# Optimization experiments

Measured on AMD Instinct MI355X. Metric: run time of the kernel, lower is better.

The kernel has to match this reference:

```python
import jax, jax.numpy as jnp
import numpy as np

DIM = 768
HEADS = 12
ROWS = COLS = 24          # 384 // 16
NP = ROWS * COLS          # 576 patches
N = NP + 1                # +1 cls token
NREL = (2 * ROWS - 1) * (2 * COLS - 1)  # 2209 relative offsets


def make_mapping_indices():
    # mapping[(di,dj)] = (di+ROWS-1)*(2*COLS-1) + (dj+COLS-1), vectorized
    i = np.arange(ROWS)[:, None, None, None]
    j = np.arange(COLS)[None, :, None, None]
    ii = np.arange(ROWS)[None, None, :, None]
    jj = np.arange(COLS)[None, None, None, :]
    idx = ((ii - i) + ROWS - 1) * (2 * COLS - 1) + ((jj - j) + COLS - 1)
    return jnp.asarray(idx.reshape(NP, NP), dtype=jnp.int32)


def setup_inputs() -> dict:
    key = jax.random.key(0)
    ks = jax.random.split(key, 7)
    B = 32
    x = jax.random.normal(ks[0], (B, N, DIM), dtype=jnp.float32)
    qkv_w = jax.random.normal(ks[1], (3 * DIM, DIM), dtype=jnp.float32) * 0.02
    proj_w = jax.random.normal(ks[2], (DIM, DIM), dtype=jnp.float32) * 0.02
    proj_b = jnp.zeros((DIM,), dtype=jnp.float32)
    beta1 = jax.random.normal(ks[3], (HEADS, 1, 1 + NP), dtype=jnp.float32) * 0.02
    beta2 = jax.random.normal(ks[4], (HEADS, NP, 1), dtype=jnp.float32) * 0.02
    beta3 = jax.random.normal(ks[5], (HEADS, NREL), dtype=jnp.float32) * 0.02
    return {"x": x, "qkv_w": qkv_w, "proj_w": proj_w, "proj_b": proj_b,
            "beta1": beta1, "beta2": beta2, "beta3": beta3,
            "mapping_indices": make_mapping_indices()}


def reference(x, qkv_w, proj_w, proj_b, beta1, beta2, beta3, mapping_indices):
    B, Nn, C = x.shape
    H = HEADS
    D = C // H
    scale = D ** -0.5
    qkv = x @ qkv_w.T                               # (B,N,3C)
    qkv = qkv.reshape(B, Nn, 3, H, D).transpose(2, 0, 3, 1, 4)
    q, k, v = qkv[0], qkv[1], qkv[2]                # (B,H,N,D)
    attn = jnp.einsum('bhid,bhjd->bhij', q, k) * scale
    # T5-style bias: (H, NP, NP) gathered rel bias + beta2 first col + beta1 last row
    rel = beta3[:, mapping_indices]                 # (H, NP, NP)
    top = jnp.concatenate([beta2, rel], axis=2)     # (H, NP, NP+1)
    beta_matrix = jnp.concatenate([top, beta1], axis=1)  # (H, N, N)
    attn = attn + beta_matrix[None]
    attn = jax.nn.softmax(attn, axis=-1)
    out = jnp.einsum('bhij,bhjd->bhid', attn, v)    # (B,H,N,D)
    out = out.transpose(0, 2, 1, 3).reshape(B, Nn, C)
    return out @ proj_w.T + proj_b
```

## Files before the change

kernel.cpp:

```cpp
#include <hip/hip_runtime.h>
#include <math.h>

#define DIMC  768
#define HEADS 12
#define NTOK  577
#define NPAT  576
#define NRELS 2209
#define BATCH 32
#define HDIM  64
#define MROWS (BATCH * NTOK)
#define NQB   5
#define NCH   10

#define AS1 __attribute__((address_space(1)))
#define AS3 __attribute__((address_space(3)))

typedef __attribute__((ext_vector_type(8))) short bf16x8;
typedef __attribute__((ext_vector_type(4))) float f32x4;
typedef __attribute__((ext_vector_type(8))) unsigned short u16x8;

__device__ __forceinline__ unsigned short f2bf(float f) {
    unsigned int u = __float_as_uint(f);
    return (unsigned short)((u + 0x7FFFu + ((u >> 16) & 1u)) >> 16);
}
__device__ __forceinline__ float bf2f(unsigned short h) {
    return __uint_as_float(((unsigned int)h) << 16);
}

__global__ __launch_bounds__(256)
void f32_to_bf16_kernel(const float* __restrict__ in, unsigned short* __restrict__ out, int n4) {
    for (int i = blockIdx.x * 256 + threadIdx.x; i < n4; i += gridDim.x * 256) {
        float4 v = reinterpret_cast<const float4*>(in)[i];
        ushort4 r;
        r.x = f2bf(v.x); r.y = f2bf(v.y); r.z = f2bf(v.z); r.w = f2bf(v.w);
        reinterpret_cast<ushort4*>(out)[i] = r;
    }
}

__global__ __launch_bounds__(256)
void build_biasF_kernel(const float* __restrict__ beta1,
                        const float* __restrict__ beta2,
                        const float* __restrict__ beta3,
                        unsigned short* __restrict__ biasF) {
    int idx = blockIdx.x * 256 + threadIdx.x;
    const int total = HEADS * NQB * NCH * 4 * 64 * 32;
    if (idx >= total) return;
    int r    = idx & 3;
    int bb   = (idx >> 2) & 3;
    int qi   = (idx >> 4) & 1;
    int lane = (idx >> 5) & 63;
    int wv   = (idx >> 11) & 3;
    int u    = idx >> 13;
    int c    = u % NCH;
    int i0b  = (u / NCH) % NQB;
    int h    = u / (NCH * NQB);
    int q = i0b * 128 + wv * 32 + qi * 16 + (lane & 15);
    int j = c * 64 + bb * 16 + ((lane >> 4) << 2) + r;
    float v;
    if (q >= NTOK || j >= NTOK) {
        v = -1e30f;
    } else if (q == NPAT) {
        v = beta1[h * NTOK + j];
    } else if (j == 0) {
        v = beta2[h * NPAT + q];
    } else {
        int p   = j - 1;
        int qi_ = q / 24, qj = q - qi_ * 24;
        int ri  = p / 24, ci = p - ri * 24;
        v = beta3[h * NRELS + (ri - qi_ + 23) * 47 + (ci - qj + 23)];
    }
    biasF[idx] = f2bf(v);
}

__global__ __launch_bounds__(256)
void vt_build_kernel(const unsigned short* __restrict__ qkv,
                     unsigned short* __restrict__ vtg) {
    __shared__ unsigned short T[64][72];
    const int c = blockIdx.x, h = blockIdx.y, b = blockIdx.z;
    const int tid = threadIdx.x;
    {
        int tok   = tid >> 2;
        int dq    = (tid & 3) << 4;
        int token = min(c * 64 + tok, NTOK - 1);
        const unsigned short* src = qkv + (size_t)(b * NTOK + token) * 2304 + 2 * DIMC + h * HDIM + dq;
        u16x8 a0 = *(const u16x8*)src;
        u16x8 a1 = *(const u16x8*)(src + 8);
        #pragma unroll
        for (int e = 0; e < 8; ++e) {
            T[dq + e][tok]     = (unsigned short)a0[e];
            T[dq + 8 + e][tok] = (unsigned short)a1[e];
        }
    }
    __syncthreads();
    {
        int d  = tid >> 2;
        int tq = (tid & 3) << 4;
        u16x8 r0 = *(const u16x8*)&T[d][tq];
        u16x8 r1 = *(const u16x8*)&T[d][tq + 8];
        unsigned short* dst = vtg + ((size_t)((b * HEADS + h) * HDIM) + d) * 640 + c * 64 + tq;
        *(u16x8*)dst       = r0;
        *(u16x8*)(dst + 8) = r1;
    }
}

template<bool ADD_BIAS, bool OUT_BF16, bool SCALE_Q>
__global__ __launch_bounds__(512, 2)
void gemm_bt_256(const unsigned short* __restrict__ A,
                 const unsigned short* __restrict__ B,
                 const float* __restrict__ bias,
                 void* __restrict__ Cv,
                 int M, int N, int K, int Mb, int Nb) {
    __shared__ __align__(16) unsigned short As[2][256 * 64];
    __shared__ __align__(16) unsigned short Bs[2][256 * 64];
    const int tid  = threadIdx.x;
    const int w    = tid >> 6;
    const int lane = tid & 63;
    const int wm   = w >> 2, wn = w & 3;
    const int l15  = lane & 15, h4 = lane >> 4;

    const int nwg  = Mb * Nb;
    const int orig = blockIdx.x;
    const int qq   = nwg >> 3, rr8 = nwg & 7;
    const int xcd  = orig & 7, loc = orig >> 3;
    const int wgid = (xcd < rr8 ? xcd * (qq + 1) : rr8 * (qq + 1) + (xcd - rr8) * qq) + loc;
    const int nblk = wgid % Nb, mblk = wgid / Nb;
    const int m0 = mblk << 8, n0 = nblk << 8;

    const int srow = tid >> 3;
    const int csrc = (tid & 7) ^ (srow & 7);
    const unsigned short* agp[4];
    const unsigned short* bgp[4];
    #pragma unroll
    for (int g = 0; g < 4; ++g) {
        int ar = min(m0 + g * 64 + srow, M - 1);
        agp[g] = A + (size_t)ar * K + csrc * 8;
        bgp[g] = B + (size_t)(n0 + g * 64 + srow) * K + csrc * 8;
    }

#define STAGE_TILE(t, buf)                                                          \
    {                                                                               \
        const int koff_ = (t) << 6;                                                 \
        _Pragma("unroll")                                                           \
        for (int g = 0; g < 4; ++g) {                                               \
            __builtin_amdgcn_global_load_lds((const AS1 void*)(agp[g] + koff_),     \
                (AS3 void*)(&As[buf][(g * 512 + tid) * 8]), 16, 0, 0);              \
            __builtin_amdgcn_global_load_lds((const AS1 void*)(bgp[g] + koff_),     \
                (AS3 void*)(&Bs[buf][(g * 512 + tid) * 8]), 16, 0, 0);              \
        }                                                                           \
    }

    f32x4 acc[8][4] = {};

    STAGE_TILE(0, 0);
    STAGE_TILE(1, 1);
    asm volatile("s_waitcnt vmcnt(8)" ::: "memory");
    __builtin_amdgcn_s_barrier();

    const int NT = K >> 6;
    for (int t = 0; t < NT; ++t) {
        const int buf = t & 1;
        bf16x8 af[2][8], bf[2][4];
        #pragma unroll
        for (int kb = 0; kb < 2; ++kb) {
            #pragma unroll
            for (int mf = 0; mf < 8; ++mf) {
                int row = wm * 128 + mf * 16 + l15;
                int ch  = (kb * 4 + h4) ^ (row & 7);
                af[kb][mf] = *(const bf16x8*)&As[buf][row * 64 + ch * 8];
            }
            #pragma unroll
            for (int nf = 0; nf < 4; ++nf) {
                int row = wn * 64 + nf * 16 + l15;
                int ch  = (kb * 4 + h4) ^ (row & 7);
                bf[kb][nf] = *(const bf16x8*)&Bs[buf][row * 64 + ch * 8];
            }
        }
        asm volatile("s_waitcnt lgkmcnt(0)" ::: "memory");
        __builtin_amdgcn_sched_barrier(0);
        __builtin_amdgcn_s_barrier();
        if (t + 2 < NT) STAGE_TILE(t + 2, buf);

        __builtin_amdgcn_s_setprio(1);
        #pragma unroll
        for (int kb = 0; kb < 2; ++kb)
            #pragma unroll
            for (int mf = 0; mf < 8; ++mf)
                #pragma unroll
                for (int nf = 0; nf < 4; ++nf)
                    acc[mf][nf] = __builtin_amdgcn_mfma_f32_16x16x32_bf16(
                        af[kb][mf], bf[kb][nf], acc[mf][nf], 0, 0, 0);
        __builtin_amdgcn_s_setprio(0);

        if (t + 2 < NT)
            asm volatile("s_waitcnt vmcnt(8)" ::: "memory");
        else if (t + 1 < NT)
            asm volatile("s_waitcnt vmcnt(0)" ::: "memory");
        __builtin_amdgcn_s_barrier();
    }
#undef STAGE_TILE

    #pragma unroll
    for (int nf = 0; nf < 4; ++nf) {
        const int col = n0 + wn * 64 + nf * 16 + l15;
        const float bv = ADD_BIAS ? bias[col] : 0.f;
        #pragma unroll
        for (int mf = 0; mf < 8; ++mf) {
            const int row0 = m0 + wm * 128 + mf * 16 + (h4 << 2);
            #pragma unroll
            for (int r = 0; r < 4; ++r) {
                int row = row0 + r;
                if (row < M) {
                    float val = acc[mf][nf][r] + bv;
                    if (SCALE_Q && col < DIMC) val *= 0.125f;
                    if (OUT_BF16)
                        ((unsigned short*)Cv)[(size_t)row * N + col] = f2bf(val);
                    else
                        ((float*)Cv)[(size_t)row * N + col] = val;
                }
            }
        }
    }
}

__global__ __launch_bounds__(256)
void attn_mfma2(const unsigned short* __restrict__ qkv,
                const unsigned short* __restrict__ vtg,
                const unsigned short* __restrict__ biasF,
                unsigned short* __restrict__ att) {
    __shared__ __align__(16) unsigned short Ks[64 * 64];
    __shared__ __align__(16) unsigned short Vs[64 * 64];
    __shared__ __align__(16) unsigned short Ps[128 * 64];

    const int b    = blockIdx.z;
    const int h    = blockIdx.y;
    const int i0b  = blockIdx.x;
    const int i0   = i0b << 7;
    const int tid  = threadIdx.x;
    const int w    = tid >> 6;
    const int lane = tid & 63;
    const int l15  = lane & 15;
    const int h4   = lane >> 4;
    const int sw   = (l15 & 7) << 3;

    bf16x8 qf[2][2];
    #pragma unroll
    for (int qi = 0; qi < 2; ++qi) {
        int qrow = min(i0 + w * 32 + qi * 16 + l15, NTOK - 1);
        const unsigned short* qp = qkv + (size_t)(b * NTOK + qrow) * 2304 + h * HDIM + h4 * 8;
        qf[qi][0] = *(const bf16x8*)qp;
        qf[qi][1] = *(const bf16x8*)(qp + 32);
    }

    const int grow   = lane >> 3;
    const int gchunk = (lane & 7) ^ grow;
    const unsigned short* kls = qkv + (size_t)b * NTOK * 2304 + DIMC + h * HDIM + gchunk * 8;
    const unsigned short* vls = vtg + (size_t)((b * HEADS + h) * HDIM) * 640 + gchunk * 8;
    const unsigned short* bias_p = biasF + ((size_t)(((h * NQB + i0b) * NCH) * 4 + w) * 64 + lane) * 32;

    float l[2] = {0.f, 0.f};
    f32x4 o[2][4] = {};

    for (int c = 0; c < NCH; ++c) {
        __syncthreads();
        #pragma unroll
        for (int t = 0; t < 2; ++t) {
            const int rbase = w * 16 + t * 8;
            const int rloc  = rbase + grow;
            const int ktok  = min(c * 64 + rloc, NTOK - 1);
            __builtin_amdgcn_global_load_lds((const AS1 void*)(kls + (size_t)ktok * 2304),
                                             (AS3 void*)(Ks + rbase * 64), 16, 0, 0);
            __builtin_amdgcn_global_load_lds((const AS1 void*)(vls + rloc * 640 + c * 64),
                                             (AS3 void*)(Vs + rbase * 64), 16, 0, 0);
        }
        u16x8 br[4];
        {
            const unsigned short* bp = bias_p + c * 8192;
            #pragma unroll
            for (int t = 0; t < 4; ++t) br[t] = *(const u16x8*)(bp + t * 8);
        }
        __syncthreads();

        __builtin_amdgcn_s_setprio(1);
        f32x4 sacc[4][2] = {};
        #pragma unroll
        for (int kb = 0; kb < 2; ++kb) {
            #pragma unroll
            for (int bb = 0; bb < 4; ++bb) {
                bf16x8 kf = *(const bf16x8*)&Ks[(bb * 16 + l15) * 64 + ((kb * 32 + h4 * 8) ^ sw)];
                sacc[bb][0] = __builtin_amdgcn_mfma_f32_16x16x32_bf16(kf, qf[0][kb], sacc[bb][0], 0, 0, 0);
                sacc[bb][1] = __builtin_amdgcn_mfma_f32_16x16x32_bf16(kf, qf[1][kb], sacc[bb][1], 0, 0, 0);
            }
        }
        __builtin_amdgcn_s_setprio(0);

        #pragma unroll
        for (int qi = 0; qi < 2; ++qi) {
            float rs = 0.f;
            #pragma unroll
            for (int bb = 0; bb < 4; ++bb) {
                const u16x8 bv = br[qi * 2 + (bb >> 1)];
                const int   e0 = (bb & 1) * 4;
                float p0 = __expf(sacc[bb][qi][0] + bf2f((unsigned short)bv[e0 + 0]));
                float p1 = __expf(sacc[bb][qi][1] + bf2f((unsigned short)bv[e0 + 1]));
                float p2 = __expf(sacc[bb][qi][2] + bf2f((unsigned short)bv[e0 + 2]));
                float p3 = __expf(sacc[bb][qi][3] + bf2f((unsigned short)bv[e0 + 3]));
                rs += (p0 + p1) + (p2 + p3);
                ushort4 pw;
                pw.x = f2bf(p0); pw.y = f2bf(p1); pw.z = f2bf(p2); pw.w = f2bf(p3);
                *(ushort4*)&Ps[(w * 32 + qi * 16 + l15) * 64 + ((bb * 16 + h4 * 4) ^ sw)] = pw;
            }
            rs += __shfl_xor(rs, 16);
            rs += __shfl_xor(rs, 32);
            l[qi] += rs;
        }

        __builtin_amdgcn_s_setprio(1);
        #pragma unroll
        for (int kb = 0; kb < 2; ++kb) {
            bf16x8 vf[4];
            #pragma unroll
            for (int nb = 0; nb < 4; ++nb)
                vf[nb] = *(const bf16x8*)&Vs[(nb * 16 + l15) * 64 + ((kb * 32 + h4 * 8) ^ sw)];
            #pragma unroll
            for (int qi = 0; qi < 2; ++qi) {
                bf16x8 pf = *(const bf16x8*)&Ps[(w * 32 + qi * 16 + l15) * 64 + ((kb * 32 + h4 * 8) ^ sw)];
                #pragma unroll
                for (int nb = 0; nb < 4; ++nb)
                    o[qi][nb] = __builtin_amdgcn_mfma_f32_16x16x32_bf16(pf, vf[nb], o[qi][nb], 0, 0, 0);
            }
        }
        __builtin_amdgcn_s_setprio(0);
    }

    #pragma unroll
    for (int qi = 0; qi < 2; ++qi) {
        #pragma unroll
        for (int r = 0; r < 4; ++r) {
            float linv = 1.0f / __shfl(l[qi], (h4 << 2) + r);
            int qrow = i0 + w * 32 + qi * 16 + (h4 << 2) + r;
            if (qrow < NTOK) {
                #pragma unroll
                for (int nb = 0; nb < 4; ++nb)
                    att[(size_t)(b * NTOK + qrow) * DIMC + h * HDIM + nb * 16 + l15] =
                        f2bf(o[qi][nb][r] * linv);
            }
        }
    }
}

extern "C" void kernel_launch(void* const* d_in, const int* in_sizes, int n_in,
                              void* d_out, int out_size, void* d_ws, size_t ws_size,
                              hipStream_t stream) {
    const float* x      = (const float*)d_in[0];
    const float* qkv_w  = (const float*)d_in[1];
    const float* proj_w = (const float*)d_in[2];
    const float* proj_b = (const float*)d_in[3];
    const float* beta1  = (const float*)d_in[4];
    const float* beta2  = (const float*)d_in[5];
    const float* beta3  = (const float*)d_in[6];
    float* out = (float*)d_out;

    unsigned short* qkvbf = (unsigned short*)d_ws;
    unsigned short* attbf = qkvbf + (size_t)MROWS * 2304;
    unsigned short* xbf   = attbf + (size_t)MROWS * DIMC;
    unsigned short* wqkv  = xbf   + (size_t)MROWS * DIMC;
    unsigned short* wproj = wqkv  + (size_t)2304 * DIMC;
    unsigned short* vtg   = wproj + (size_t)DIMC * DIMC;
    unsigned short* biasF = vtg   + (size_t)BATCH * HEADS * HDIM * 640;

    f32_to_bf16_kernel<<<2048, 256, 0, stream>>>(x, xbf, MROWS * DIMC / 4);
    f32_to_bf16_kernel<<<1024, 256, 0, stream>>>(qkv_w, wqkv, 2304 * DIMC / 4);
    f32_to_bf16_kernel<<<512, 256, 0, stream>>>(proj_w, wproj, DIMC * DIMC / 4);

    build_biasF_kernel<<<(HEADS * NQB * NCH * 4 * 64 * 32 + 255) / 256, 256, 0, stream>>>(
        beta1, beta2, beta3, biasF);

    {
        const int Mb = (MROWS + 255) / 256, Nb = (3 * DIMC) / 256;
        gemm_bt_256<false, true, true><<<Mb * Nb, 512, 0, stream>>>(
            xbf, wqkv, nullptr, qkvbf, MROWS, 3 * DIMC, DIMC, Mb, Nb);
    }
    {
        dim3 g(NCH, HEADS, BATCH);
        vt_build_kernel<<<g, 256, 0, stream>>>(qkvbf, vtg);
    }
    {
        dim3 g(NQB, HEADS, BATCH);
        attn_mfma2<<<g, 256, 0, stream>>>(qkvbf, vtg, biasF, attbf);
    }
    {
        const int Mb = (MROWS + 255) / 256, Nb = DIMC / 256;
        gemm_bt_256<true, false, false><<<Mb * Nb, 512, 0, stream>>>(
            attbf, wproj, proj_b, out, MROWS, DIMC, DIMC, Mb, Nb);
    }
}
```

Baseline: 375.0 us.

## Restructure GEMM into 8-phase half-tile pipeline with LDS-staged coalesced epilogue

Replaces the double-buffered 256x256 GEMM loop with an 8-phase schedule. Each 64-wide K step is split into A and B halves loaded separately, and fragment reads are interleaved with MFMA quarter-blocks so that global-to-LDS loads, LDS reads and MFMAs overlap more finely. The epilogue now writes the accumulators through a swizzled LDS scratch buffer and emits vectorized, coalesced 16-byte row stores instead of scattered scalar stores. The cost is many more barriers per iteration and tighter vmcnt accounting, which could stall waves or become fragile if the load counts change.

```diff
diff --git a/kernel.cpp b/kernel.cpp
--- a/kernel.cpp
+++ b/kernel.cpp
@@ -105,18 +105,18 @@
 
 template<bool ADD_BIAS, bool OUT_BF16, bool SCALE_Q>
 __global__ __launch_bounds__(512, 2)
-void gemm_bt_256(const unsigned short* __restrict__ A,
-                 const unsigned short* __restrict__ B,
-                 const float* __restrict__ bias,
-                 void* __restrict__ Cv,
-                 int M, int N, int K, int Mb, int Nb) {
-    __shared__ __align__(16) unsigned short As[2][256 * 64];
-    __shared__ __align__(16) unsigned short Bs[2][256 * 64];
+void gemm_8ph(const unsigned short* __restrict__ A,
+              const unsigned short* __restrict__ B,
+              const float* __restrict__ bias,
+              void* __restrict__ Cv,
+              int M, int N, int K, int Mb, int Nb) {
+    __shared__ __align__(16) unsigned short SM[65536];
     const int tid  = threadIdx.x;
     const int w    = tid >> 6;
     const int lane = tid & 63;
     const int wm   = w >> 2, wn = w & 3;
     const int l15  = lane & 15, h4 = lane >> 4;
+    const int bh   = wn >> 1, bsub = (wn & 1) << 6;
 
     const int nwg  = Mb * Nb;
     const int orig = blockIdx.x;
@@ -126,97 +126,133 @@
     const int nblk = wgid % Nb, mblk = wgid / Nb;
     const int m0 = mblk << 8, n0 = nblk << 8;
 
-    const int srow = tid >> 3;
-    const int csrc = (tid & 7) ^ (srow & 7);
-    const unsigned short* agp[4];
-    const unsigned short* bgp[4];
+    const int r0 = tid >> 3;
+    const int cs = (((tid & 7) ^ (r0 & 7)) << 3);
+    const unsigned short* ap[2][2];
+    const unsigned short* bp[2][2];
     #pragma unroll
-    for (int g = 0; g < 4; ++g) {
-        int ar = min(m0 + g * 64 + srow, M - 1);
-        agp[g] = A + (size_t)ar * K + csrc * 8;
-        bgp[g] = B + (size_t)(n0 + g * 64 + srow) * K + csrc * 8;
-    }
-
-#define STAGE_TILE(t, buf)                                                          \
-    {                                                                               \
-        const int koff_ = (t) << 6;                                                 \
-        _Pragma("unroll")                                                           \
-        for (int g = 0; g < 4; ++g) {                                               \
-            __builtin_amdgcn_global_load_lds((const AS1 void*)(agp[g] + koff_),     \
-                (AS3 void*)(&As[buf][(g * 512 + tid) * 8]), 16, 0, 0);              \
-            __builtin_amdgcn_global_load_lds((const AS1 void*)(bgp[g] + koff_),     \
-                (AS3 void*)(&Bs[buf][(g * 512 + tid) * 8]), 16, 0, 0);              \
-        }                                                                           \
-    }
+    for (int h = 0; h < 2; ++h)
+        #pragma unroll
+        for (int j = 0; j < 2; ++j) {
+            ap[h][j] = A + (size_t)min(m0 + h * 128 + j * 64 + r0, M - 1) * K + cs;
+            bp[h][j] = B + (size_t)(n0 + h * 128 + j * 64 + r0) * K + cs;
+        }
+
+#define GLL(src, dst) __builtin_amdgcn_global_load_lds((const AS1 void*)(src), (AS3 void*)(dst), 16, 0, 0)
+#define ADST(d, h, j) (SM + ((d) * 2 + (h)) * 8192 + (j) * 4096 + (w << 9))
+#define BDST(d, h, j) (SM + 32768 + ((d) * 2 + (h)) * 8192 + (j) * 4096 + (w << 9))
+#define STAGE_A(d, koff) { GLL(ap[0][0] + (koff), ADST(d,0,0)); GLL(ap[0][1] + (koff), ADST(d,0,1)); \
+                           GLL(ap[1][0] + (koff), ADST(d,1,0)); GLL(ap[1][1] + (koff), ADST(d,1,1)); }
+#define STAGE_B(d, koff) { GLL(bp[0][0] + (koff), BDST(d,0,0)); GLL(bp[0][1] + (koff), BDST(d,0,1)); \
+                           GLL(bp[1][0] + (koff), BDST(d,1,0)); GLL(bp[1][1] + (koff), BDST(d,1,1)); }
+
+    const int chk0 = ((h4) ^ (l15 & 7)) << 3;
+    const int chk1 = ((4 + h4) ^ (l15 & 7)) << 3;
+#define RD_A(d, mh) { _Pragma("unroll") for (int mf4 = 0; mf4 < 4; ++mf4) { \
+        const unsigned short* rp = SM + ((d) * 2 + wm) * 8192 + (((mh) * 64 + mf4 * 16 + l15) << 6); \
+        af[0][mf4] = *(const bf16x8*)(rp + chk0); af[1][mf4] = *(const bf16x8*)(rp + chk1); } }
+#define RD_B(d, nh, dst) { _Pragma("unroll") for (int nf2 = 0; nf2 < 2; ++nf2) { \
+        const unsigned short* rp = SM + 32768 + ((d) * 2 + bh) * 8192 + ((bsub + (nh) * 32 + nf2 * 16 + l15) << 6); \
+        dst[0][nf2] = *(const bf16x8*)(rp + chk0); dst[1][nf2] = *(const bf16x8*)(rp + chk1); } }
+#define MMA(mh, nh, afr, bfr) { __builtin_amdgcn_s_setprio(1); \
+        _Pragma("unroll") for (int kb = 0; kb < 2; ++kb) \
+        _Pragma("unroll") for (int mf4 = 0; mf4 < 4; ++mf4) \
+        _Pragma("unroll") for (int nf2 = 0; nf2 < 2; ++nf2) \
+            acc[(mh) * 4 + mf4][(nh) * 2 + nf2] = __builtin_amdgcn_mfma_f32_16x16x32_bf16( \
+                afr[kb][mf4], bfr[kb][nf2], acc[(mh) * 4 + mf4][(nh) * 2 + nf2], 0, 0, 0); \
+        __builtin_amdgcn_s_setprio(0); }
+#define BARR  __builtin_amdgcn_s_barrier()
+#define LGKM0 { asm volatile("s_waitcnt lgkmcnt(0)" ::: "memory"); __builtin_amdgcn_sched_barrier(0); }
+#define VM4   asm volatile("s_waitcnt vmcnt(4)" ::: "memory")
+#define VM0   asm volatile("s_waitcnt vmcnt(0)" ::: "memory")
 
     f32x4 acc[8][4] = {};
 
-    STAGE_TILE(0, 0);
-    STAGE_TILE(1, 1);
-    asm volatile("s_waitcnt vmcnt(8)" ::: "memory");
-    __builtin_amdgcn_s_barrier();
-
-    const int NT = K >> 6;
-    for (int t = 0; t < NT; ++t) {
-        const int buf = t & 1;
-        bf16x8 af[2][8], bf[2][4];
-        #pragma unroll
-        for (int kb = 0; kb < 2; ++kb) {
-            #pragma unroll
-            for (int mf = 0; mf < 8; ++mf) {
-                int row = wm * 128 + mf * 16 + l15;
-                int ch  = (kb * 4 + h4) ^ (row & 7);
-                af[kb][mf] = *(const bf16x8*)&As[buf][row * 64 + ch * 8];
-            }
-            #pragma unroll
-            for (int nf = 0; nf < 4; ++nf) {
-                int row = wn * 64 + nf * 16 + l15;
-                int ch  = (kb * 4 + h4) ^ (row & 7);
-                bf[kb][nf] = *(const bf16x8*)&Bs[buf][row * 64 + ch * 8];
-            }
-        }
-        asm volatile("s_waitcnt lgkmcnt(0)" ::: "memory");
-        __builtin_amdgcn_sched_barrier(0);
-        __builtin_amdgcn_s_barrier();
-        if (t + 2 < NT) STAGE_TILE(t + 2, buf);
-
-        __builtin_amdgcn_s_setprio(1);
-        #pragma unroll
-        for (int kb = 0; kb < 2; ++kb)
-            #pragma unroll
-            for (int mf = 0; mf < 8; ++mf)
+    STAGE_A(0, 0); STAGE_B(0, 0); STAGE_A(1, 64);
+    VM4; BARR;
+
+    const int NIT = K >> 7;
+    for (int it = 0; it < NIT; ++it) {
+        const int k0 = it << 7;
+        const bool more = (it + 1 < NIT);
+        bf16x8 af[2][4], bfA[2][2], bfB[2][2];
+        RD_A(0, 0); RD_B(0, 0, bfA);
+        STAGE_B(1, k0 + 64);
+        BARR; LGKM0; MMA(0, 0, af, bfA); BARR;
+
+        RD_B(0, 1, bfB);
+        BARR; LGKM0; MMA(0, 1, af, bfB); BARR;
+
+        RD_A(0, 1);
+        BARR; LGKM0; MMA(1, 1, af, bfB); BARR;
+
+        if (more) STAGE_A(0, k0 + 128);
+        BARR; MMA(1, 0, af, bfA);
+        if (more) { VM4; } else { VM0; }
+        BARR;
+        RD_A(1, 0); RD_B(1, 0, bfA);
+        if (more) STAGE_B(0, k0 + 128);
+        BARR; LGKM0; MMA(0, 0, af, bfA); BARR;
+
+        RD_B(1, 1, bfB);
+        BARR; LGKM0; MMA(0, 1, af, bfB); BARR;
+
+        RD_A(1, 1);
+        BARR; LGKM0; MMA(1, 1, af, bfB); BARR;
+
+        if (more) STAGE_A(1, k0 + 192);
+        BARR; MMA(1, 0, af, bfA);
+        if (more) { VM4; } else { VM0; }
+        BARR;
+    }
+#undef STAGE_A
+#undef STAGE_B
+
+    BARR;
+    float* scr = (float*)SM + (w << 12);
+    const int rowbase = m0 + wm * 128;
+    const int colbase = n0 + wn * 64;
+    #pragma unroll
+    for (int pass = 0; pass < 2; ++pass) {
+        #pragma unroll
+        for (int mf4 = 0; mf4 < 4; ++mf4)
+            #pragma unroll
+            for (int nf = 0; nf < 4; ++nf)
                 #pragma unroll
-                for (int nf = 0; nf < 4; ++nf)
-                    acc[mf][nf] = __builtin_amdgcn_mfma_f32_16x16x32_bf16(
-                        af[kb][mf], bf[kb][nf], acc[mf][nf], 0, 0, 0);
-        __builtin_amdgcn_s_setprio(0);
-
-        if (t + 2 < NT)
-            asm volatile("s_waitcnt vmcnt(8)" ::: "memory");
-        else if (t + 1 < NT)
-            asm volatile("s_waitcnt vmcnt(0)" ::: "memory");
-        __builtin_amdgcn_s_barrier();
-    }
-#undef STAGE_TILE
-
-    #pragma unroll
-    for (int nf = 0; nf < 4; ++nf) {
-        const int col = n0 + wn * 64 + nf * 16 + l15;
-        const float bv = ADD_BIAS ? bias[col] : 0.f;
-        #pragma unroll
-        for (int mf = 0; mf < 8; ++mf) {
-            const int row0 = m0 + wm * 128 + mf * 16 + (h4 << 2);
-            #pragma unroll
-            for (int r = 0; r < 4; ++r) {
-                int row = row0 + r;
-                if (row < M) {
-                    float val = acc[mf][nf][r] + bv;
-                    if (SCALE_Q && col < DIMC) val *= 0.125f;
-                    if (OUT_BF16)
-                        ((unsigned short*)Cv)[(size_t)row * N + col] = f2bf(val);
-                    else
-                        ((float*)Cv)[(size_t)row * N + col] = val;
+                for (int r = 0; r < 4; ++r) {
+                    int row = mf4 * 16 + (h4 << 2) + r;
+                    int col = nf * 16 + l15;
+                    float v = acc[pass * 4 + mf4][nf][r];
+                    int gcol = colbase + col;
+                    if (ADD_BIAS) v += bias[gcol];
+                    if (SCALE_Q && gcol < DIMC) v *= 0.125f;
+                    scr[(row << 6) + (col ^ ((row & 7) << 3))] = v;
                 }
+        if (OUT_BF16) {
+            const int rr = lane >> 3, c8 = (lane & 7) << 3;
+            #pragma unroll
+            for (int k8 = 0; k8 < 8; ++k8) {
+                int row = rr + k8 * 8;
+                int p = (row << 6) + (c8 ^ ((row & 7) << 3));
+                f32x4 v0 = *(const f32x4*)&scr[p];
+                f32x4 v1 = *(const f32x4*)&scr[p + 4];
+                int grow = rowbase + pass * 64 + row;
+                if (grow < M) {
+                    u16x8 o;
+                    o[0] = f2bf(v0[0]); o[1] = f2bf(v0[1]); o[2] = f2bf(v0[2]); o[3] = f2bf(v0[3]);
+                    o[4] = f2bf(v1[0]); o[5] = f2bf(v1[1]); o[6] = f2bf(v1[2]); o[7] = f2bf(v1[3]);
+                    *(u16x8*)((unsigned short*)Cv + (size_t)grow * N + colbase + c8) = o;
+                }
+            }
+        } else {
+            const int rr = lane >> 4, c4 = (lane & 15) << 2;
+            #pragma unroll
+            for (int k4 = 0; k4 < 16; ++k4) {
+                int row = rr + k4 * 4;
+                f32x4 v = *(const f32x4*)&scr[(row << 6) + (c4 ^ ((row & 7) << 3))];
+                int grow = rowbase + pass * 64 + row;
+                if (grow < M)
+                    *(f32x4*)((float*)Cv + (size_t)grow * N + colbase + c4) = v;
             }
         }
     }
@@ -377,7 +413,7 @@
 
     {
         const int Mb = (MROWS + 255) / 256, Nb = (3 * DIMC) / 256;
-        gemm_bt_256<false, true, true><<<Mb * Nb, 512, 0, stream>>>(
+        gemm_8ph<false, true, true><<<Mb * Nb, 512, 0, stream>>>(
             xbf, wqkv, nullptr, qkvbf, MROWS, 3 * DIMC, DIMC, Mb, Nb);
     }
     {
@@ -390,7 +426,7 @@
     }
     {
         const int Mb = (MROWS + 255) / 256, Nb = DIMC / 256;
-        gemm_bt_256<true, false, false><<<Mb * Nb, 512, 0, stream>>>(
+        gemm_8ph<true, false, false><<<Mb * Nb, 512, 0, stream>>>(
             attbf, wproj, proj_b, out, MROWS, DIMC, DIMC, Mb, Nb);
     }
 }
```

Result: faster. 340.0 us (-9.3%).

## Shrink GEMM tiles to 128x128 and stage epilogue through LDS for coalesced stores

Applied to the files above, without the earlier changes.

Replaces the 256x256, 512-thread GEMM with a 128x128, 256-thread version, quadrupling the number of workgroups to improve load balance across CUs. The epilogue now writes accumulators into swizzled LDS scratch and then emits vectorised row-contiguous global stores (8 bf16 or 4 fp32 per thread) instead of scattered scalar stores. Smaller tiles reduce data reuse per block and the scratch spans past As into Bs.

```diff
diff --git a/kernel.cpp b/kernel.cpp
--- a/kernel.cpp
+++ b/kernel.cpp
@@ -104,18 +104,18 @@
 }
 
 template<bool ADD_BIAS, bool OUT_BF16, bool SCALE_Q>
-__global__ __launch_bounds__(512, 2)
-void gemm_bt_256(const unsigned short* __restrict__ A,
-                 const unsigned short* __restrict__ B,
-                 const float* __restrict__ bias,
-                 void* __restrict__ Cv,
-                 int M, int N, int K, int Mb, int Nb) {
-    __shared__ __align__(16) unsigned short As[2][256 * 64];
-    __shared__ __align__(16) unsigned short Bs[2][256 * 64];
+__global__ __launch_bounds__(256, 2)
+void gemm_128(const unsigned short* __restrict__ A,
+              const unsigned short* __restrict__ B,
+              const float* __restrict__ bias,
+              void* __restrict__ Cv,
+              int M, int N, int K, int Mb, int Nb) {
+    __shared__ __align__(16) unsigned short As[2][128 * 64];
+    __shared__ __align__(16) unsigned short Bs[2][128 * 64];
     const int tid  = threadIdx.x;
     const int w    = tid >> 6;
     const int lane = tid & 63;
-    const int wm   = w >> 2, wn = w & 3;
+    const int wm   = w >> 1, wn = w & 1;
     const int l15  = lane & 15, h4 = lane >> 4;
 
     const int nwg  = Mb * Nb;
@@ -124,32 +124,30 @@
     const int xcd  = orig & 7, loc = orig >> 3;
     const int wgid = (xcd < rr8 ? xcd * (qq + 1) : rr8 * (qq + 1) + (xcd - rr8) * qq) + loc;
     const int nblk = wgid % Nb, mblk = wgid / Nb;
-    const int m0 = mblk << 8, n0 = nblk << 8;
-
-    const int srow = tid >> 3;
-    const int csrc = (tid & 7) ^ (srow & 7);
-    const unsigned short* agp[4];
-    const unsigned short* bgp[4];
+    const int m0 = mblk << 7, n0 = nblk << 7;
+
+    const int r0 = tid >> 3;
+    const int cs = (((tid & 7) ^ (r0 & 7)) << 3);
+    const unsigned short* ap[4];
+    const unsigned short* bp[4];
     #pragma unroll
     for (int g = 0; g < 4; ++g) {
-        int ar = min(m0 + g * 64 + srow, M - 1);
-        agp[g] = A + (size_t)ar * K + csrc * 8;
-        bgp[g] = B + (size_t)(n0 + g * 64 + srow) * K + csrc * 8;
-    }
-
-#define STAGE_TILE(t, buf)                                                          \
-    {                                                                               \
-        const int koff_ = (t) << 6;                                                 \
-        _Pragma("unroll")                                                           \
-        for (int g = 0; g < 4; ++g) {                                               \
-            __builtin_amdgcn_global_load_lds((const AS1 void*)(agp[g] + koff_),     \
-                (AS3 void*)(&As[buf][(g * 512 + tid) * 8]), 16, 0, 0);              \
-            __builtin_amdgcn_global_load_lds((const AS1 void*)(bgp[g] + koff_),     \
-                (AS3 void*)(&Bs[buf][(g * 512 + tid) * 8]), 16, 0, 0);              \
-        }                                                                           \
-    }
-
-    f32x4 acc[8][4] = {};
+        ap[g] = A + (size_t)min(m0 + g * 32 + r0, M - 1) * K + cs;
+        bp[g] = B + (size_t)(n0 + g * 32 + r0) * K + cs;
+    }
+
+#define GLL(src, dst) __builtin_amdgcn_global_load_lds((const AS1 void*)(src), (AS3 void*)(dst), 16, 0, 0)
+#define STAGE_TILE(t, buf)                                                  \
+    {                                                                       \
+        const int koff_ = (t) << 6;                                         \
+        _Pragma("unroll")                                                   \
+        for (int g = 0; g < 4; ++g) {                                       \
+            GLL(ap[g] + koff_, &As[buf][(g * 256 + tid) * 8]);              \
+            GLL(bp[g] + koff_, &Bs[buf][(g * 256 + tid) * 8]);              \
+        }                                                                   \
+    }
+
+    f32x4 acc[4][4] = {};
 
     STAGE_TILE(0, 0);
     STAGE_TILE(1, 1);
@@ -159,12 +157,12 @@
     const int NT = K >> 6;
     for (int t = 0; t < NT; ++t) {
         const int buf = t & 1;
-        bf16x8 af[2][8], bf[2][4];
+        bf16x8 af[2][4], bf[2][4];
         #pragma unroll
         for (int kb = 0; kb < 2; ++kb) {
             #pragma unroll
-            for (int mf = 0; mf < 8; ++mf) {
-                int row = wm * 128 + mf * 16 + l15;
+            for (int mf = 0; mf < 4; ++mf) {
+                int row = wm * 64 + mf * 16 + l15;
                 int ch  = (kb * 4 + h4) ^ (row & 7);
                 af[kb][mf] = *(const bf16x8*)&As[buf][row * 64 + ch * 8];
             }
@@ -184,7 +182,7 @@
         #pragma unroll
         for (int kb = 0; kb < 2; ++kb)
             #pragma unroll
-            for (int mf = 0; mf < 8; ++mf)
+            for (int mf = 0; mf < 4; ++mf)
                 #pragma unroll
                 for (int nf = 0; nf < 4; ++nf)
                     acc[mf][nf] = __builtin_amdgcn_mfma_f32_16x16x32_bf16(
@@ -198,26 +196,51 @@
         __builtin_amdgcn_s_barrier();
     }
 #undef STAGE_TILE
-
+#undef GLL
+
+    __builtin_amdgcn_s_barrier();
+    float* scr = (float*)As + (w << 12);
+    const int rowbase = m0 + wm * 64;
+    const int colbase = n0 + wn * 64;
     #pragma unroll
-    for (int nf = 0; nf < 4; ++nf) {
-        const int col = n0 + wn * 64 + nf * 16 + l15;
-        const float bv = ADD_BIAS ? bias[col] : 0.f;
-        #pragma unroll
-        for (int mf = 0; mf < 8; ++mf) {
-            const int row0 = m0 + wm * 128 + mf * 16 + (h4 << 2);
+    for (int mf = 0; mf < 4; ++mf)
+        #pragma unroll
+        for (int nf = 0; nf < 4; ++nf)
             #pragma unroll
             for (int r = 0; r < 4; ++r) {
-                int row = row0 + r;
-                if (row < M) {
-                    float val = acc[mf][nf][r] + bv;
-                    if (SCALE_Q && col < DIMC) val *= 0.125f;
-                    if (OUT_BF16)
-                        ((unsigned short*)Cv)[(size_t)row * N + col] = f2bf(val);
-                    else
-                        ((float*)Cv)[(size_t)row * N + col] = val;
-                }
-            }
+                int row = mf * 16 + (h4 << 2) + r;
+                int col = nf * 16 + l15;
+                float v = acc[mf][nf][r];
+                int gcol = colbase + col;
+                if (ADD_BIAS) v += bias[gcol];
+                if (SCALE_Q && gcol < DIMC) v *= 0.125f;
+                scr[(row << 6) + (col ^ ((row & 7) << 3))] = v;
+            }
+    if (OUT_BF16) {
+        const int rr = lane >> 3, c8 = (lane & 7) << 3;
+        #pragma unroll
+        for (int k8 = 0; k8 < 8; ++k8) {
+            int row = k8 * 8 + rr;
+            int p = (row << 6) + (c8 ^ ((row & 7) << 3));
+            f32x4 v0 = *(const f32x4*)&scr[p];
+            f32x4 v1 = *(const f32x4*)&scr[p + 4];
+            int grow = rowbase + row;
+            if (grow < M) {
+                u16x8 o;
+                o[0] = f2bf(v0[0]); o[1] = f2bf(v0[1]); o[2] = f2bf(v0[2]); o[3] = f2bf(v0[3]);
+                o[4] = f2bf(v1[0]); o[5] = f2bf(v1[1]); o[6] = f2bf(v1[2]); o[7] = f2bf(v1[3]);
+                *(u16x8*)((unsigned short*)Cv + (size_t)grow * N + colbase + c8) = o;
+            }
+        }
+    } else {
+        const int rr = lane >> 4, c4 = (lane & 15) << 2;
+        #pragma unroll
+        for (int k4 = 0; k4 < 16; ++k4) {
+            int row = k4 * 4 + rr;
+            f32x4 v = *(const f32x4*)&scr[(row << 6) + (c4 ^ ((row & 7) << 3))];
+            int grow = rowbase + row;
+            if (grow < M)
+                *(f32x4*)((float*)Cv + (size_t)grow * N + colbase + c4) = v;
         }
     }
 }
@@ -376,8 +399,8 @@
         beta1, beta2, beta3, biasF);
 
     {
-        const int Mb = (MROWS + 255) / 256, Nb = (3 * DIMC) / 256;
-        gemm_bt_256<false, true, true><<<Mb * Nb, 512, 0, stream>>>(
+        const int Mb = (MROWS + 127) / 128, Nb = (3 * DIMC) / 128;
+        gemm_128<false, true, true><<<Mb * Nb, 256, 0, stream>>>(
             xbf, wqkv, nullptr, qkvbf, MROWS, 3 * DIMC, DIMC, Mb, Nb);
     }
     {
@@ -389,8 +412,8 @@
         attn_mfma2<<<g, 256, 0, stream>>>(qkvbf, vtg, biasF, attbf);
     }
     {
-        const int Mb = (MROWS + 255) / 256, Nb = DIMC / 256;
-        gemm_bt_256<true, false, false><<<Mb * Nb, 512, 0, stream>>>(
+        const int Mb = (MROWS + 127) / 128, Nb = DIMC / 128;
+        gemm_128<true, false, false><<<Mb * Nb, 256, 0, stream>>>(
             attbf, wproj, proj_b, out, MROWS, DIMC, DIMC, Mb, Nb);
     }
 }
```

Measured after the change: 355.1 us. 5.3% less time.
